# Kernel tuning notes

Measured on AMD Instinct MI355X. Metric: run time of the kernel, lower is better.

Reference implementation:

```python
import jax, jax.numpy as jnp
import numpy as np

N_EMBD = 1024
N_HEAD = 16
HEAD_SIZE = N_EMBD // N_HEAD  # 64


def rotate_half(x):
    x1, x2 = x[..., : x.shape[-1] // 2], x[..., x.shape[-1] // 2 :]
    return jnp.concatenate([-x2, x1], axis=-1)


def rope_cos_sin(T, head_size, dtype):
    inv_freq = 1.0 / (10000.0 ** (jnp.arange(0, head_size, 2, dtype=jnp.float32) / head_size))
    t = jnp.arange(T, dtype=jnp.float32)
    freqs = jnp.outer(t, inv_freq)  # (T, D/2)
    emb = jnp.concatenate([freqs, freqs], axis=-1)  # (T, D)
    return jnp.cos(emb).astype(dtype), jnp.sin(emb).astype(dtype)


def setup_inputs() -> dict:
    key = jax.random.key(0)
    k1, k2, k3, k4 = jax.random.split(key, 4)
    B, T, C = 4, 4096, N_EMBD
    scale = 1.0 / np.sqrt(C)
    return {
        "x": jax.random.normal(k1, (B, T, C), dtype=jnp.float32),
        "sigma0": jnp.zeros((B, N_HEAD, HEAD_SIZE, HEAD_SIZE), dtype=jnp.float32),
        "w_qkv": jax.random.normal(k2, (3 * C, C), dtype=jnp.float32) * scale,
        "w_proj": jax.random.normal(k3, (C, C), dtype=jnp.float32) * scale,
        "eta": jnp.ones((1,), dtype=jnp.float32) * 0.1,
    }


def reference(x, sigma0, w_qkv, w_proj, eta):
    B, T, C = x.shape
    H, D = N_HEAD, HEAD_SIZE
    qkv = x @ w_qkv.T  # (B,T,3C)
    q, k, v = jnp.split(qkv, 3, axis=-1)
    # (B,T,C) -> (B,H,T,D)
    q = q.reshape(B, T, H, D).transpose(0, 2, 1, 3)
    k = k.reshape(B, T, H, D).transpose(0, 2, 1, 3)
    v = v.reshape(B, T, H, D).transpose(0, 2, 1, 3)
    cos, sin = rope_cos_sin(T, D, x.dtype)  # (T,D) broadcast over (B,H,T,D)
    q = q * cos + rotate_half(q) * sin
    k = k * cos + rotate_half(k) * sin
    q = jax.nn.relu(q)
    k = jax.nn.relu(k)
    # sequential Hebbian fast-weight scan over time
    q_t = q.transpose(2, 0, 1, 3)  # (T,B,H,D)
    k_t = k.transpose(2, 0, 1, 3)
    v_t = v.transpose(2, 0, 1, 3)
    eta_s = eta[0]

    def step(sigma, qkv_step):
        qt, kt, vt = qkv_step  # each (B,H,D)
        out_t = jnp.einsum("bhd,bhde->bhe", qt, sigma)  # read BEFORE update
        sigma = sigma + eta_s * jnp.einsum("bhd,bhe->bhde", kt, vt)
        return sigma, out_t

    sigma_final, outs = jax.lax.scan(step, sigma0, (q_t, k_t, v_t))
    # outs: (T,B,H,D) -> (B,T,C)
    out = outs.transpose(1, 0, 2, 3).reshape(B, T, C)
    out = out @ w_proj.T
    return out, sigma_final
```

## Files before the change

kernel.cpp:

```cpp
#include <hip/hip_runtime.h>
#include <hip/hip_bf16.h>
#include <cstdint>
#include <cstddef>

#define B_   4
#define T_   4096
#define C_   1024
#define H_   16
#define NC_  64
#define M_   (B_*T_)
#define N3_  (3*C_)
#define NTK  16

typedef __attribute__((ext_vector_type(4))) float  f32x4;
typedef __attribute__((ext_vector_type(8))) __bf16 bf16x8;
typedef __attribute__((ext_vector_type(4))) __bf16 bf16x4;
typedef __attribute__((ext_vector_type(8))) unsigned short u16x8;

__device__ __forceinline__ void glds16(void* lds, const void* g) {
  __builtin_amdgcn_global_load_lds((const __attribute__((address_space(1))) void*)g,
                                   (__attribute__((address_space(3))) void*)lds,
                                   16, 0, 0);
}
#define MFMA_BF16 __builtin_amdgcn_mfma_f32_16x16x32_bf16

__global__ __launch_bounds__(256) void cvt_f32_bf16(const float* __restrict__ in,
                                                    __bf16* __restrict__ out, int n4) {
  int i = blockIdx.x * 256 + threadIdx.x;
  if (i >= n4) return;
  float4 v = reinterpret_cast<const float4*>(in)[i];
  bf16x4 o;
  o[0] = (__bf16)v.x; o[1] = (__bf16)v.y; o[2] = (__bf16)v.z; o[3] = (__bf16)v.w;
  reinterpret_cast<bf16x4*>(out)[i] = o;
}

__global__ __launch_bounds__(256) void rope_tab(float2* __restrict__ tab) {
  int gid = blockIdx.x * 256 + threadIdx.x;
  int t = gid >> 5, dp = gid & 31;
  float invf = exp2f(-(float)dp * (13.287712379549449f / 32.0f));
  float ang = (float)t * invf;
  float s, c;
  sincosf(ang, &s, &c);
  tab[gid] = make_float2(c, s);
}

template<int FUSE>
__global__ __launch_bounds__(512) void gemm_dbuf(const __bf16* __restrict__ A,
                                                 const __bf16* __restrict__ Bt,
                                                 void* __restrict__ Cout,
                                                 const float2* __restrict__ tab,
                                                 int N) {
  __shared__ __bf16 sA[2][256 * 64];
  __shared__ __bf16 sB[2][256 * 64];
  const int tid  = threadIdx.x;
  const int lane = tid & 63;
  const int wave = tid >> 6;
  const int wm = wave >> 2, wn = wave & 3;
  const int bm = blockIdx.y, bn = blockIdx.x;
  const int fr = lane & 15, kq = lane >> 4;
  const int fr7 = fr & 7;
  const int K = C_;

  const int r_loc = tid >> 3;
  const int sslot = (tid & 7) ^ (r_loc & 7);
  const __bf16* Ag = A  + (size_t)(bm * 256 + r_loc) * K + sslot * 8;
  const __bf16* Bg = Bt + (size_t)(bn * 256 + r_loc) * K + sslot * 8;

  f32x4 acc[8][4];
#pragma unroll
  for (int i = 0; i < 8; i++)
#pragma unroll
    for (int j = 0; j < 4; j++) acc[i][j] = (f32x4)0.0f;

#pragma unroll
  for (int q = 0; q < 4; ++q) {
    glds16((char*)sA[0] + q * 8192 + tid * 16, Ag + (size_t)q * 64 * K);
    glds16((char*)sB[0] + q * 8192 + tid * 16, Bg + (size_t)q * 64 * K);
  }
  asm volatile("s_waitcnt vmcnt(0)" ::: "memory");
  __builtin_amdgcn_sched_barrier(0);
  __builtin_amdgcn_s_barrier();

  bf16x8 af[4][2], bfr[4][2];
  for (int t = 0; t < NTK; ++t) {
    const int buf = t & 1, nb = buf ^ 1;
    const __bf16* Ab = (const __bf16*)sA[buf];
    const __bf16* Bb = (const __bf16*)sB[buf];

    if (t + 1 < NTK) {
      const int kb = (t + 1) * 64;
#pragma unroll
      for (int q = 0; q < 4; ++q) {
        glds16((char*)sA[nb] + q * 8192 + tid * 16, Ag + (size_t)q * 64 * K + kb);
        glds16((char*)sB[nb] + q * 8192 + tid * 16, Bg + (size_t)q * 64 * K + kb);
      }
    }

#pragma unroll
    for (int j = 0; j < 4; ++j)
#pragma unroll
      for (int kk = 0; kk < 2; ++kk)
        bfr[j][kk] = *(const bf16x8*)((const char*)Bb + (wn * 64 + j * 16 + fr) * 128 +
                                      (((kk << 2) | kq) ^ fr7) * 16);
#pragma unroll
    for (int h = 0; h < 2; ++h) {
#pragma unroll
      for (int i = 0; i < 4; ++i)
#pragma unroll
        for (int kk = 0; kk < 2; ++kk)
          af[i][kk] = *(const bf16x8*)((const char*)Ab +
                        (wm * 128 + (h * 4 + i) * 16 + fr) * 128 +
                        (((kk << 2) | kq) ^ fr7) * 16);
      __builtin_amdgcn_s_setprio(1);
#pragma unroll
      for (int i = 0; i < 4; ++i)
#pragma unroll
        for (int j = 0; j < 4; ++j) {
          acc[h * 4 + i][j] = MFMA_BF16(af[i][0], bfr[j][0], acc[h * 4 + i][j], 0, 0, 0);
          acc[h * 4 + i][j] = MFMA_BF16(af[i][1], bfr[j][1], acc[h * 4 + i][j], 0, 0, 0);
        }
      __builtin_amdgcn_s_setprio(0);
    }

    if (t < NTK - 1) {
      asm volatile("s_waitcnt vmcnt(0)" ::: "memory");
      __builtin_amdgcn_sched_barrier(0);
      __builtin_amdgcn_s_barrier();
    }
  }

  const int rg4 = kq * 4;
  const int cb = bn * 256 + wn * 64;
  if (FUSE == 1 && bn < 8) {
#pragma unroll
    for (int i = 0; i < 8; ++i)
#pragma unroll
      for (int r = 0; r < 4; ++r) {
        size_t row = (size_t)bm * 256 + wm * 128 + i * 16 + rg4 + r;
        int tt = (int)(row & (T_ - 1));
#pragma unroll
        for (int j = 0; j < 2; ++j) {
          int dp = j * 16 + fr;
          float2 cs = tab[tt * 32 + dp];
          float x1 = acc[i][j][r], x2 = acc[i][j + 2][r];
          float o1 = fmaxf(x1 * cs.x - x2 * cs.y, 0.0f);
          float o2 = fmaxf(x2 * cs.x + x1 * cs.y, 0.0f);
          ((__bf16*)Cout)[row * N + cb + j * 16 + fr]      = (__bf16)o1;
          ((__bf16*)Cout)[row * N + cb + j * 16 + fr + 32] = (__bf16)o2;
        }
      }
  } else {
#pragma unroll
    for (int i = 0; i < 8; ++i)
#pragma unroll
      for (int j = 0; j < 4; ++j) {
        size_t row = (size_t)bm * 256 + wm * 128 + i * 16 + rg4;
        size_t col = (size_t)cb + j * 16 + fr;
#pragma unroll
        for (int r = 0; r < 4; ++r) {
          if (FUSE == 2) ((float*)Cout)[(row + r) * N + col]  = acc[i][j][r];
          else           ((__bf16*)Cout)[(row + r) * N + col] = (__bf16)acc[i][j][r];
        }
      }
  }
}

#define LDW 72
__global__ __launch_bounds__(256) void chunk_kv(const __bf16* __restrict__ qkv,
                                                __bf16* __restrict__ G) {
  __shared__ __bf16 Kt[64 * LDW];
  __shared__ __bf16 Vt[64 * LDW];
  const int bid = blockIdx.x;
  const int c = bid & (NC_ - 1);
  const int bh = bid >> 6;
  const int h = bh & (H_ - 1);
  const int b = bh >> 4;
  const int tid = threadIdx.x;
  const size_t row0 = (size_t)b * T_ + c * 64;
  const int kcol = C_ + h * 64;
  const int vcol = 2 * C_ + h * 64;
#pragma unroll
  for (int it = 0; it < 2; ++it) {
    int task = tid + it * 256;
    int t = task >> 3;
    int d0 = (task & 7) * 8;
    const size_t rb = (row0 + t) * N3_;
    u16x8 kv = *(const u16x8*)(qkv + rb + kcol + d0);
    u16x8 vv = *(const u16x8*)(qkv + rb + vcol + d0);
#pragma unroll
    for (int j = 0; j < 8; j++) {
      ((unsigned short*)Kt)[(d0 + j) * LDW + t] = kv[j];
      ((unsigned short*)Vt)[(d0 + j) * LDW + t] = vv[j];
    }
  }
  __syncthreads();
  const int lane = tid & 63, wave = tid >> 6;
  const int gr = (wave >> 1) * 32, gc = (wave & 1) * 32;
  const int fr = lane & 15, kb = (lane >> 4) * 8;
  f32x4 acc[2][2];
#pragma unroll
  for (int i = 0; i < 2; i++)
#pragma unroll
    for (int j = 0; j < 2; j++) acc[i][j] = (f32x4)0.0f;
#pragma unroll
  for (int kk = 0; kk < 2; ++kk) {
    bf16x8 af[2], bfr[2];
#pragma unroll
    for (int i = 0; i < 2; i++)
      af[i] = *(const bf16x8*)(Kt + (gr + i * 16 + fr) * LDW + kk * 32 + kb);
#pragma unroll
    for (int j = 0; j < 2; j++)
      bfr[j] = *(const bf16x8*)(Vt + (gc + j * 16 + fr) * LDW + kk * 32 + kb);
#pragma unroll
    for (int i = 0; i < 2; i++)
#pragma unroll
      for (int j = 0; j < 2; j++)
        acc[i][j] = MFMA_BF16(af[i], bfr[j], acc[i][j], 0, 0, 0);
  }
  const int rg = (lane >> 4) * 4;
  __bf16* Gb = G + (size_t)bid * 4096;
#pragma unroll
  for (int i = 0; i < 2; i++)
#pragma unroll
    for (int j = 0; j < 2; j++)
#pragma unroll
      for (int r = 0; r < 4; r++)
        Gb[(gr + i * 16 + rg + r) * 64 + gc + j * 16 + fr] = (__bf16)acc[i][j][r];
}

__global__ __launch_bounds__(256) void prefix_scan(const __bf16* __restrict__ G,
                                                   const float* __restrict__ sigma0,
                                                   __bf16* __restrict__ S,
                                                   float* __restrict__ sigma_out,
                                                   const float* __restrict__ eta) {
  const int blk = blockIdx.x;
  const int bh = blk >> 2;
  const int dq = blk & 3;
  const int tid = threadIdx.x;
  const int d = dq * 16 + (tid >> 4);
  const int e0 = (tid & 15) * 4;
  const float eta_s = eta[0];
  const size_t base_de = (size_t)d * 64 + e0;
  float acc[4], s0[4];
#pragma unroll
  for (int j = 0; j < 4; j++) {
    acc[j] = 0.0f;
    s0[j] = sigma0[(size_t)bh * 4096 + base_de + j];
  }
  for (int c = 0; c < NC_; ++c) {
    const size_t off = ((size_t)bh * NC_ + c) * 4096 + base_de;
    bf16x4 sv;
#pragma unroll
    for (int j = 0; j < 4; j++) sv[j] = (__bf16)(s0[j] + eta_s * acc[j]);
    *(bf16x4*)(S + off) = sv;
    bf16x4 g = *(const bf16x4*)(G + off);
#pragma unroll
    for (int j = 0; j < 4; j++) acc[j] += (float)g[j];
  }
  float4 v;
  v.x = s0[0] + eta_s * acc[0];
  v.y = s0[1] + eta_s * acc[1];
  v.z = s0[2] + eta_s * acc[2];
  v.w = s0[3] + eta_s * acc[3];
  *reinterpret_cast<float4*>(sigma_out + (size_t)bh * 4096 + base_de) = v;
}

__global__ __launch_bounds__(256) void chunk_out(const __bf16* __restrict__ qkv,
                                                 const __bf16* __restrict__ S,
                                                 __bf16* __restrict__ outp,
                                                 const float* __restrict__ eta) {
  __shared__ __bf16 Qs[64 * LDW];
  __shared__ __bf16 Ks[64 * LDW];
  __shared__ __bf16 Vt[64 * LDW];
  __shared__ __bf16 St[64 * LDW];
  __shared__ __bf16 Ps[64 * LDW];
  const int bid = blockIdx.x;
  const int c = bid & 63, bh = bid >> 6, h = bh & 15, b = bh >> 4;
  const int tid = threadIdx.x;
  const size_t row0 = (size_t)b * T_ + c * 64;
  const float eta_s = eta[0];
#pragma unroll
  for (int it = 0; it < 2; ++it) {
    int task = tid + it * 256;
    int t = task >> 3, d0 = (task & 7) * 8;
    const size_t rb = (row0 + t) * N3_;
    *(u16x8*)(Qs + t * LDW + d0) = *(const u16x8*)(qkv + rb + h * 64 + d0);
    *(u16x8*)(Ks + t * LDW + d0) = *(const u16x8*)(qkv + rb + C_ + h * 64 + d0);
    u16x8 vv = *(const u16x8*)(qkv + rb + 2 * C_ + h * 64 + d0);
    u16x8 sv = *(const u16x8*)(S + (size_t)bid * 4096 + t * 64 + d0);
#pragma unroll
    for (int j = 0; j < 8; j++) {
      ((unsigned short*)Vt)[(d0 + j) * LDW + t] = vv[j];
      ((unsigned short*)St)[(d0 + j) * LDW + t] = sv[j];
    }
  }
  __syncthreads();
  const int lane = tid & 63, wave = tid >> 6;
  const int qr = (wave >> 1) * 32, qc = (wave & 1) * 32;
  const int fr = lane & 15, kb = (lane >> 4) * 8, rg = (lane >> 4) * 4;
  {
    f32x4 pacc[2][2];
#pragma unroll
    for (int i = 0; i < 2; i++)
#pragma unroll
      for (int j = 0; j < 2; j++) pacc[i][j] = (f32x4)0.0f;
#pragma unroll
    for (int kk = 0; kk < 2; ++kk) {
      bf16x8 af[2], bfr[2];
#pragma unroll
      for (int i = 0; i < 2; i++)
        af[i] = *(const bf16x8*)(Qs + (qr + i * 16 + fr) * LDW + kk * 32 + kb);
#pragma unroll
      for (int j = 0; j < 2; j++)
        bfr[j] = *(const bf16x8*)(Ks + (qc + j * 16 + fr) * LDW + kk * 32 + kb);
#pragma unroll
      for (int i = 0; i < 2; i++)
#pragma unroll
        for (int j = 0; j < 2; j++)
          pacc[i][j] = MFMA_BF16(af[i], bfr[j], pacc[i][j], 0, 0, 0);
    }
#pragma unroll
    for (int i = 0; i < 2; i++)
#pragma unroll
      for (int j = 0; j < 2; j++)
#pragma unroll
        for (int r = 0; r < 4; r++) {
          int trow = qr + i * 16 + rg + r;
          int scol = qc + j * 16 + fr;
          float v = (scol < trow) ? eta_s * pacc[i][j][r] : 0.0f;
          Ps[trow * LDW + scol] = (__bf16)v;
        }
  }
  __syncthreads();
  {
    f32x4 oacc[2][2];
#pragma unroll
    for (int i = 0; i < 2; i++)
#pragma unroll
      for (int j = 0; j < 2; j++) oacc[i][j] = (f32x4)0.0f;
#pragma unroll
    for (int kk = 0; kk < 2; ++kk) {
      bf16x8 pa[2], vb[2], qa[2], sb[2];
#pragma unroll
      for (int i = 0; i < 2; i++) {
        pa[i] = *(const bf16x8*)(Ps + (qr + i * 16 + fr) * LDW + kk * 32 + kb);
        qa[i] = *(const bf16x8*)(Qs + (qr + i * 16 + fr) * LDW + kk * 32 + kb);
      }
#pragma unroll
      for (int j = 0; j < 2; j++) {
        vb[j] = *(const bf16x8*)(Vt + (qc + j * 16 + fr) * LDW + kk * 32 + kb);
        sb[j] = *(const bf16x8*)(St + (qc + j * 16 + fr) * LDW + kk * 32 + kb);
      }
#pragma unroll
      for (int i = 0; i < 2; i++)
#pragma unroll
        for (int j = 0; j < 2; j++) {
          oacc[i][j] = MFMA_BF16(pa[i], vb[j], oacc[i][j], 0, 0, 0);
          oacc[i][j] = MFMA_BF16(qa[i], sb[j], oacc[i][j], 0, 0, 0);
        }
    }
#pragma unroll
    for (int i = 0; i < 2; i++)
#pragma unroll
      for (int j = 0; j < 2; j++)
#pragma unroll
        for (int r = 0; r < 4; r++) {
          size_t row = row0 + qr + i * 16 + rg + r;
          int col = h * 64 + qc + j * 16 + fr;
          outp[row * C_ + col] = (__bf16)oacc[i][j][r];
        }
  }
}

extern "C" void kernel_launch(void* const* d_in, const int* in_sizes, int n_in,
                              void* d_out, int out_size, void* d_ws, size_t ws_size,
                              hipStream_t stream) {
  const float* x      = (const float*)d_in[0];
  const float* sigma0 = (const float*)d_in[1];
  const float* w_qkv  = (const float*)d_in[2];
  const float* w_proj = (const float*)d_in[3];
  const float* eta    = (const float*)d_in[4];
  float* out       = (float*)d_out;
  float* sigma_out = out + (size_t)M_ * C_;

  char* ws = (char*)d_ws;
  __bf16* xbf     = (__bf16*)(ws);
  __bf16* wqkvbf  = (__bf16*)(ws + 33554432);
  __bf16* wprojbf = (__bf16*)(ws + 39845888);
  __bf16* qkvbf   = (__bf16*)(ws + 41943040);
  __bf16* Gws     = (__bf16*)(ws + 142606336);
  __bf16* Sws     = (__bf16*)(ws + 176160768);
  float2* tab     = (float2*)(ws + 176160768);

  rope_tab<<<512, 256, 0, stream>>>(tab);
  cvt_f32_bf16<<<16384, 256, 0, stream>>>(x, xbf, 4194304);
  cvt_f32_bf16<<<3072, 256, 0, stream>>>(w_qkv, wqkvbf, 786432);
  cvt_f32_bf16<<<1024, 256, 0, stream>>>(w_proj, wprojbf, 262144);
  gemm_dbuf<1><<<dim3(12, 64), 512, 0, stream>>>(xbf, wqkvbf, (void*)qkvbf, tab, N3_);
  chunk_kv<<<4096, 256, 0, stream>>>(qkvbf, Gws);
  prefix_scan<<<256, 256, 0, stream>>>(Gws, sigma0, Sws, sigma_out, eta);
  chunk_out<<<4096, 256, 0, stream>>>(qkvbf, Sws, xbf, eta);
  gemm_dbuf<2><<<dim3(4, 64), 512, 0, stream>>>(xbf, wprojbf, (void*)out, nullptr, C_);
}
```

Measured before the change: 267.7 us.

## Restructure GEMM main loop into phased quadrant schedule with interleaved staging

Replaces the double-buffered GEMM loop with an 8-phase schedule modeled on the HipKittens design. Each K-tile is split into four quadrant MFMA blocks, and the global-to-LDS loads for the next tile are spread across those phases with barriers and fine-grained waitcnts. This aims to overlap memory staging with MFMA work and shrink per-wave fragment register pressure. It adds many more block barriers per iteration, which could cost throughput. The correctness of the wave-to-quadrant mapping and the vmcnt accounting is subtle.

```diff
diff --git a/kernel.cpp b/kernel.cpp
--- a/kernel.cpp
+++ b/kernel.cpp
@@ -45,13 +45,13 @@
 }
 
 template<int FUSE>
-__global__ __launch_bounds__(512) void gemm_dbuf(const __bf16* __restrict__ A,
-                                                 const __bf16* __restrict__ Bt,
-                                                 void* __restrict__ Cout,
-                                                 const float2* __restrict__ tab,
-                                                 int N) {
-  __shared__ __bf16 sA[2][256 * 64];
-  __shared__ __bf16 sB[2][256 * 64];
+__global__ __launch_bounds__(512) void gemm_8ph(const __bf16* __restrict__ A,
+                                               const __bf16* __restrict__ Bt,
+                                               void* __restrict__ Cout,
+                                               const float2* __restrict__ tab,
+                                               int N) {
+  __shared__ __bf16 sA[2][2][128 * 64];
+  __shared__ __bf16 sB[2][2][128 * 64];
   const int tid  = threadIdx.x;
   const int lane = tid & 63;
   const int wave = tid >> 6;
@@ -73,60 +73,119 @@
     for (int j = 0; j < 4; j++) acc[i][j] = (f32x4)0.0f;
 
 #pragma unroll
-  for (int q = 0; q < 4; ++q) {
-    glds16((char*)sA[0] + q * 8192 + tid * 16, Ag + (size_t)q * 64 * K);
-    glds16((char*)sB[0] + q * 8192 + tid * 16, Bg + (size_t)q * 64 * K);
-  }
-  asm volatile("s_waitcnt vmcnt(0)" ::: "memory");
-  __builtin_amdgcn_sched_barrier(0);
-  __builtin_amdgcn_s_barrier();
+  for (int h = 0; h < 2; ++h)
+#pragma unroll
+    for (int q = 0; q < 2; ++q) {
+      glds16((char*)sA[0][h] + q * 8192 + tid * 16, Ag + (size_t)(h * 128 + q * 64) * K);
+      glds16((char*)sB[0][h] + q * 8192 + tid * 16, Bg + (size_t)(h * 128 + q * 64) * K);
+    }
+
+  const __bf16* AgH[2] = { Ag, Ag + (size_t)128 * K };
+  const __bf16* BgH[2] = { Bg, Bg + (size_t)128 * K };
 
   bf16x8 af[4][2], bfr[4][2];
+  const int bloc = (wn & 1) * 64;
+
   for (int t = 0; t < NTK; ++t) {
-    const int buf = t & 1, nb = buf ^ 1;
-    const __bf16* Ab = (const __bf16*)sA[buf];
-    const __bf16* Bb = (const __bf16*)sB[buf];
-
-    if (t + 1 < NTK) {
-      const int kb = (t + 1) * 64;
-#pragma unroll
-      for (int q = 0; q < 4; ++q) {
-        glds16((char*)sA[nb] + q * 8192 + tid * 16, Ag + (size_t)q * 64 * K + kb);
-        glds16((char*)sB[nb] + q * 8192 + tid * 16, Bg + (size_t)q * 64 * K + kb);
-      }
-    }
-
-#pragma unroll
-    for (int j = 0; j < 4; ++j)
+    const int d = t & 1, nb = d ^ 1;
+    const bool dostage = (t + 1 < NTK);
+    const int kb1 = (t + 1) * 64;
+    const char* Abh = (const char*)sA[d][wm];
+    const char* Bbh = (const char*)sB[d][wn >> 1];
+
+    if (dostage) {
+      glds16((char*)sA[nb][0] +    0 + tid * 16, AgH[0] + kb1);
+      glds16((char*)sA[nb][0] + 8192 + tid * 16, AgH[0] + (size_t)64 * K + kb1);
+      asm volatile("s_waitcnt vmcnt(2)" ::: "memory");
+    } else {
+      asm volatile("s_waitcnt vmcnt(0)" ::: "memory");
+    }
+    __builtin_amdgcn_sched_barrier(0);
+    __builtin_amdgcn_s_barrier();
+#pragma unroll
+    for (int i = 0; i < 4; ++i)
 #pragma unroll
       for (int kk = 0; kk < 2; ++kk)
-        bfr[j][kk] = *(const bf16x8*)((const char*)Bb + (wn * 64 + j * 16 + fr) * 128 +
-                                      (((kk << 2) | kq) ^ fr7) * 16);
-#pragma unroll
-    for (int h = 0; h < 2; ++h) {
-#pragma unroll
-      for (int i = 0; i < 4; ++i)
-#pragma unroll
-        for (int kk = 0; kk < 2; ++kk)
-          af[i][kk] = *(const bf16x8*)((const char*)Ab +
-                        (wm * 128 + (h * 4 + i) * 16 + fr) * 128 +
-                        (((kk << 2) | kq) ^ fr7) * 16);
-      __builtin_amdgcn_s_setprio(1);
-#pragma unroll
-      for (int i = 0; i < 4; ++i)
-#pragma unroll
-        for (int j = 0; j < 4; ++j) {
-          acc[h * 4 + i][j] = MFMA_BF16(af[i][0], bfr[j][0], acc[h * 4 + i][j], 0, 0, 0);
-          acc[h * 4 + i][j] = MFMA_BF16(af[i][1], bfr[j][1], acc[h * 4 + i][j], 0, 0, 0);
-        }
-      __builtin_amdgcn_s_setprio(0);
-    }
-
-    if (t < NTK - 1) {
-      asm volatile("s_waitcnt vmcnt(0)" ::: "memory");
-      __builtin_amdgcn_sched_barrier(0);
-      __builtin_amdgcn_s_barrier();
-    }
+        af[i][kk] = *(const bf16x8*)(Abh + (i * 16 + fr) * 128 + (((kk << 2) | kq) ^ fr7) * 16);
+#pragma unroll
+    for (int j = 0; j < 2; ++j)
+#pragma unroll
+      for (int kk = 0; kk < 2; ++kk)
+        bfr[j][kk] = *(const bf16x8*)(Bbh + (bloc + j * 16 + fr) * 128 + (((kk << 2) | kq) ^ fr7) * 16);
+    asm volatile("s_waitcnt lgkmcnt(0)" ::: "memory");
+    __builtin_amdgcn_sched_barrier(0);
+    __builtin_amdgcn_s_setprio(1);
+#pragma unroll
+    for (int i = 0; i < 4; ++i)
+#pragma unroll
+      for (int j = 0; j < 2; ++j) {
+        acc[i][j] = MFMA_BF16(af[i][0], bfr[j][0], acc[i][j], 0, 0, 0);
+        acc[i][j] = MFMA_BF16(af[i][1], bfr[j][1], acc[i][j], 0, 0, 0);
+      }
+    __builtin_amdgcn_s_setprio(0);
+    __builtin_amdgcn_s_barrier();
+
+#pragma unroll
+    for (int j = 0; j < 2; ++j)
+#pragma unroll
+      for (int kk = 0; kk < 2; ++kk)
+        bfr[j + 2][kk] = *(const bf16x8*)(Bbh + (bloc + (j + 2) * 16 + fr) * 128 + (((kk << 2) | kq) ^ fr7) * 16);
+    if (dostage) {
+      glds16((char*)sA[nb][1] +    0 + tid * 16, AgH[1] + kb1);
+      glds16((char*)sA[nb][1] + 8192 + tid * 16, AgH[1] + (size_t)64 * K + kb1);
+    }
+    __builtin_amdgcn_s_barrier();
+    asm volatile("s_waitcnt lgkmcnt(0)" ::: "memory");
+    __builtin_amdgcn_sched_barrier(0);
+    __builtin_amdgcn_s_setprio(1);
+#pragma unroll
+    for (int i = 0; i < 4; ++i)
+#pragma unroll
+      for (int j = 0; j < 2; ++j) {
+        acc[i][j + 2] = MFMA_BF16(af[i][0], bfr[j + 2][0], acc[i][j + 2], 0, 0, 0);
+        acc[i][j + 2] = MFMA_BF16(af[i][1], bfr[j + 2][1], acc[i][j + 2], 0, 0, 0);
+      }
+    __builtin_amdgcn_s_setprio(0);
+    __builtin_amdgcn_s_barrier();
+
+#pragma unroll
+    for (int i = 0; i < 4; ++i)
+#pragma unroll
+      for (int kk = 0; kk < 2; ++kk)
+        af[i][kk] = *(const bf16x8*)(Abh + (64 + i * 16 + fr) * 128 + (((kk << 2) | kq) ^ fr7) * 16);
+    if (dostage) {
+      glds16((char*)sB[nb][0] +    0 + tid * 16, BgH[0] + kb1);
+      glds16((char*)sB[nb][0] + 8192 + tid * 16, BgH[0] + (size_t)64 * K + kb1);
+    }
+    __builtin_amdgcn_s_barrier();
+    asm volatile("s_waitcnt lgkmcnt(0)" ::: "memory");
+    __builtin_amdgcn_sched_barrier(0);
+    __builtin_amdgcn_s_setprio(1);
+#pragma unroll
+    for (int i = 0; i < 4; ++i)
+#pragma unroll
+      for (int j = 0; j < 2; ++j) {
+        acc[i + 4][j] = MFMA_BF16(af[i][0], bfr[j][0], acc[i + 4][j], 0, 0, 0);
+        acc[i + 4][j] = MFMA_BF16(af[i][1], bfr[j][1], acc[i + 4][j], 0, 0, 0);
+      }
+    __builtin_amdgcn_s_setprio(0);
+    __builtin_amdgcn_s_barrier();
+
+    if (dostage) {
+      glds16((char*)sB[nb][1] +    0 + tid * 16, BgH[1] + kb1);
+      glds16((char*)sB[nb][1] + 8192 + tid * 16, BgH[1] + (size_t)64 * K + kb1);
+    }
+    __builtin_amdgcn_s_barrier();
+    __builtin_amdgcn_s_setprio(1);
+#pragma unroll
+    for (int i = 0; i < 4; ++i)
+#pragma unroll
+      for (int j = 0; j < 2; ++j) {
+        acc[i + 4][j + 2] = MFMA_BF16(af[i][0], bfr[j + 2][0], acc[i + 4][j + 2], 0, 0, 0);
+        acc[i + 4][j + 2] = MFMA_BF16(af[i][1], bfr[j + 2][1], acc[i + 4][j + 2], 0, 0, 0);
+      }
+    __builtin_amdgcn_s_setprio(0);
+    __builtin_amdgcn_s_barrier();
   }
 
   const int rg4 = kq * 4;
@@ -396,9 +455,9 @@
   cvt_f32_bf16<<<16384, 256, 0, stream>>>(x, xbf, 4194304);
   cvt_f32_bf16<<<3072, 256, 0, stream>>>(w_qkv, wqkvbf, 786432);
   cvt_f32_bf16<<<1024, 256, 0, stream>>>(w_proj, wprojbf, 262144);
-  gemm_dbuf<1><<<dim3(12, 64), 512, 0, stream>>>(xbf, wqkvbf, (void*)qkvbf, tab, N3_);
+  gemm_8ph<1><<<dim3(12, 64), 512, 0, stream>>>(xbf, wqkvbf, (void*)qkvbf, tab, N3_);
   chunk_kv<<<4096, 256, 0, stream>>>(qkvbf, Gws);
   prefix_scan<<<256, 256, 0, stream>>>(Gws, sigma0, Sws, sigma_out, eta);
   chunk_out<<<4096, 256, 0, stream>>>(qkvbf, Sws, xbf, eta);
-  gemm_dbuf<2><<<dim3(4, 64), 512, 0, stream>>>(xbf, wprojbf, (void*)out, nullptr, C_);
-}
+  gemm_8ph<2><<<dim3(4, 64), 512, 0, stream>>>(xbf, wprojbf, (void*)out, nullptr, C_);
+}
```

Result: no change. 269.3 us (+0.6%).
